# Optimization experiments

Measured on AMD Instinct MI355X. Metric: run time of the kernel, lower is better.

Reference implementation:

```python
import jax, jax.numpy as jnp
import numpy as np

NEG = -1e30  # log-space 'zero'


def setup_inputs() -> dict:
    key = jax.random.key(0)
    T, B, C, L = 1000, 32, 2000, 100
    k1, k2 = jax.random.split(key)
    activations = jax.random.normal(k1, (T, B, C), dtype=jnp.float32)
    # targets cannot be blank (blank == 0) -> sample in [1, C)
    targets = jax.random.randint(k2, (B * L,), 1, C, dtype=jnp.int32)
    input_lengths = jnp.full((B,), T, dtype=jnp.int32)
    target_lengths = jnp.full((B,), L, dtype=jnp.int32)
    return {"activations": activations, "targets": targets,
            "input_lengths": input_lengths, "target_lengths": target_lengths}


def _ctc_costs(activations, targets, input_lengths, target_lengths, blank=0):
    """Per-utterance CTC negative log likelihoods via the alpha DP recursion."""
    T, B, C = activations.shape
    L = targets.shape[0] // B  # equal label lengths per utterance (concatenated flat)
    S = 2 * L + 1              # extended label sequence: blank-interleaved
    lp = jax.nn.log_softmax(activations, axis=-1)  # [T,B,C]
    tgt = targets.reshape(B, L)
    ext = jnp.full((B, S), blank, dtype=tgt.dtype).at[:, 1::2].set(tgt)  # [B,S]
    # log-prob of each extended-label symbol at each frame: [T,B,S]
    lp_ext = jnp.take_along_axis(lp, jnp.broadcast_to(ext[None], (T, B, S)), axis=2)
    # skip transition s-2 -> s allowed iff ext[s] != blank and ext[s] != ext[s-2]
    ext_m2 = jnp.concatenate([jnp.full((B, 2), -1, ext.dtype), ext[:, :-2]], axis=1)
    skip = (ext != blank) & (ext != ext_m2)  # [B,S]

    alpha0 = (jnp.full((B, S), NEG, jnp.float32)
              .at[:, 0].set(lp_ext[0, :, 0])
              .at[:, 1].set(lp_ext[0, :, 1]))

    def step(alpha, lp_t):
        a1 = jnp.concatenate([jnp.full((B, 1), NEG, alpha.dtype), alpha[:, :-1]], axis=1)
        a2 = jnp.concatenate([jnp.full((B, 2), NEG, alpha.dtype), alpha[:, :-2]], axis=1)
        a2 = jnp.where(skip, a2, NEG)
        m = jnp.maximum(jnp.maximum(alpha, a1), a2)
        new = m + jnp.log(jnp.exp(alpha - m) + jnp.exp(a1 - m) + jnp.exp(a2 - m)) + lp_t
        return new, new

    _, alphas = jax.lax.scan(step, alpha0, lp_ext[1:])
    alphas = jnp.concatenate([alpha0[None], alphas], axis=0)  # [T,B,S]
    # alpha at the last valid frame of each utterance
    alpha_fin = alphas[input_lengths - 1, jnp.arange(B)]  # [B,S]
    s_last = (2 * target_lengths).astype(jnp.int32)  # final blank position
    a_b = jnp.take_along_axis(alpha_fin, s_last[:, None], axis=1)[:, 0]
    a_l = jnp.take_along_axis(alpha_fin, (s_last - 1)[:, None], axis=1)[:, 0]
    m = jnp.maximum(a_b, a_l)
    return -(m + jnp.log(jnp.exp(a_b - m) + jnp.exp(a_l - m)))  # [B]


def reference(activations, targets, input_lengths, target_lengths):
    # warp-ctc 'mean' reduction: sum(costs) / minibatch / sum(target_lengths)
    costs = _ctc_costs(activations, targets, input_lengths, target_lengths, blank=0)
    B = costs.shape[0]
    return jnp.sum(costs) / B / jnp.sum(target_lengths).astype(jnp.float32)
```

## Files before the change

### kernel.cpp

```cpp
#include <hip/hip_runtime.h>
#include <math.h>


#define BLK 256

__global__ __launch_bounds__(BLK) void k_lse_gather(
    const float* __restrict__ act, const int* __restrict__ targets,
    float* __restrict__ p_ext, int T, int B, int C, int L, int S)
{
  int row = blockIdx.x;
  int b = row % B;
  int t = row / B;
  int tid = threadIdx.x;
  const float* rp = act + (size_t)row * (size_t)C;
  const float4* rp4 = (const float4*)rp;
  int C4 = C >> 2;

  float4 x0 = (tid < C4) ? rp4[tid] : make_float4(-3e38f, -3e38f, -3e38f, -3e38f);
  bool h2 = (tid + BLK) < C4;
  float4 x1 = h2 ? rp4[tid + BLK] : make_float4(0.f, 0.f, 0.f, 0.f);
  float m = fmaxf(fmaxf(x0.x, x0.y), fmaxf(x0.z, x0.w));
  if (h2) m = fmaxf(m, fmaxf(fmaxf(x1.x, x1.y), fmaxf(x1.z, x1.w)));
  for (int i = tid + 2 * BLK; i < C4; i += BLK) {
    float4 x = rp4[i];
    m = fmaxf(m, fmaxf(fmaxf(x.x, x.y), fmaxf(x.z, x.w)));
  }
  #pragma unroll
  for (int o = 32; o > 0; o >>= 1) m = fmaxf(m, __shfl_xor(m, o));
  __shared__ float sm[BLK / 64];
  __shared__ float ss[BLK / 64];
  int w = tid >> 6, ln = tid & 63;
  if (ln == 0) sm[w] = m;
  __syncthreads();
  float M = fmaxf(fmaxf(sm[0], sm[1]), fmaxf(sm[2], sm[3]));

  float ssum = 0.f;
  if (tid < C4)
    ssum += expf(x0.x - M) + expf(x0.y - M) + expf(x0.z - M) + expf(x0.w - M);
  if (h2)
    ssum += expf(x1.x - M) + expf(x1.y - M) + expf(x1.z - M) + expf(x1.w - M);
  for (int i = tid + 2 * BLK; i < C4; i += BLK) {
    float4 x = rp4[i];
    ssum += expf(x.x - M) + expf(x.y - M) + expf(x.z - M) + expf(x.w - M);
  }
  #pragma unroll
  for (int o = 32; o > 0; o >>= 1) ssum += __shfl_xor(ssum, o);
  if (ln == 0) ss[w] = ssum;
  __syncthreads();
  float lse = M + logf(ss[0] + ss[1] + ss[2] + ss[3]);

  float* op = p_ext + ((size_t)b * T + t) * 256;
  float p = 0.f;
  if (tid < S) {
    int c = (tid & 1) ? targets[b * L + (tid >> 1)] : 0;
    p = expf(rp[c] - lse);
  }
  op[tid] = p;
}

__device__ __forceinline__ float wave_max64(float x) {
  int t;
  t = __builtin_amdgcn_update_dpp(0, __float_as_int(x), 0x111, 0xF, 0xF, true);
  x = fmaxf(x, __int_as_float(t));
  t = __builtin_amdgcn_update_dpp(0, __float_as_int(x), 0x112, 0xF, 0xF, true);
  x = fmaxf(x, __int_as_float(t));
  t = __builtin_amdgcn_update_dpp(0, __float_as_int(x), 0x114, 0xF, 0xF, true);
  x = fmaxf(x, __int_as_float(t));
  t = __builtin_amdgcn_update_dpp(0, __float_as_int(x), 0x118, 0xF, 0xF, true);
  x = fmaxf(x, __int_as_float(t));
  t = __builtin_amdgcn_update_dpp(0, __float_as_int(x), 0x142, 0xA, 0xF, false);
  x = fmaxf(x, __int_as_float(t));
  t = __builtin_amdgcn_update_dpp(0, __float_as_int(x), 0x143, 0xC, 0xF, false);
  x = fmaxf(x, __int_as_float(t));
  return __int_as_float(__builtin_amdgcn_readlane(__float_as_int(x), 63));
}

__device__ __forceinline__ float shift_up1(float x) {
  int t = __builtin_amdgcn_update_dpp(0, __float_as_int(x), 0x138, 0xF, 0xF, true);
  return __int_as_float(t);
}

__global__ __launch_bounds__(64, 1) void k_alpha(
    const float* __restrict__ p_ext, const int* __restrict__ targets,
    const int* __restrict__ ilen, const int* __restrict__ tlen,
    double* __restrict__ costs, int T, int B, int L)
{
  int b = blockIdx.x;
  int l = threadIdx.x;
  int Tb = ilen[b];
  int Lb = tlen[b];
  int S = 2 * Lb + 1;

  const float4* pb4 = (const float4*)(p_ext + (size_t)b * (size_t)T * 256);

  const int* tg = targets + b * L;
  float kf3 = 0.f, kf5 = 0.f, kf7 = 0.f;
  {
    int s;
    s = 4 * l - 1; if (s >= 3 && s < S) { int mm = (s - 1) >> 1; kf3 = (tg[mm] != tg[mm - 1]) ? 1.f : 0.f; }
    s = 4 * l + 1; if (s >= 3 && s < S) { int mm = (s - 1) >> 1; kf5 = (tg[mm] != tg[mm - 1]) ? 1.f : 0.f; }
    s = 4 * l + 3; if (s >= 3 && s < S) { int mm = (s - 1) >> 1; kf7 = (tg[mm] != tg[mm - 1]) ? 1.f : 0.f; }
  }

  const float BIAS = 18446744073709551616.0f;
  float a0 = 0.f, a1 = 0.f, a2 = 0.f, a3 = 0.f;
  {
    float4 p0 = pb4[l];
    if (l == 0) { a0 = p0.x * BIAS; a1 = p0.y * BIAS; }
  }
  int E = -64;

  int i0 = (l == 0) ? 0 : (l - 1);

  const int PF = 8;
  int NE = (Tb - 1) >> 1;
  int tmax = T - 2;
  float4 fa[PF], fb[PF], fc[PF];
  #pragma unroll
  for (int j = 0; j < PF; j++) {
    int t0 = 1 + 2 * j;
    t0 = (t0 > tmax) ? tmax : t0;
    fa[j] = pb4[(size_t)t0 * 64 + i0];
    fb[j] = pb4[(size_t)t0 * 64 + l];
    fc[j] = pb4[(size_t)(t0 + 1) * 64 + l];
  }

  int e = 0;
  while (e < NE) {
    #pragma unroll
    for (int j = 0; j < PF; j++) {
      int eg = e + j;
      if (eg < NE) {
        float4 Pa = fa[j], Pb = fb[j], Pc = fc[j];
        {
          int tn = 1 + 2 * (eg + PF);
          tn = (tn > tmax) ? tmax : tn;
          fa[j] = pb4[(size_t)tn * 64 + i0];
          fb[j] = pb4[(size_t)tn * 64 + l];
          fc[j] = pb4[(size_t)(tn + 1) * 64 + l];
        }

        float w0 = shift_up1(a0), w1 = shift_up1(a1);
        float w2 = shift_up1(a2), w3 = shift_up1(a3);
        float w4 = a0, w5 = a1, w6 = a2, w7 = a3;

        w7 = (w7 + w6 + kf7 * w5) * Pb.w;
        w6 = (w6 + w5) * Pb.z;
        w5 = (w5 + w4 + kf5 * w3) * Pb.y;
        w4 = (w4 + w3) * Pb.x;
        w3 = (w3 + w2 + kf3 * w1) * Pa.w;
        w2 = (w2 + w1) * Pa.z;
        w7 = (w7 + w6 + kf7 * w5) * Pc.w;
        w6 = (w6 + w5) * Pc.z;
        w5 = (w5 + w4 + kf5 * w3) * Pc.y;
        w4 = (w4 + w3) * Pc.x;
        a0 = w4; a1 = w5; a2 = w6; a3 = w7;

        if ((j & 1) == 1) {
          float mx = fmaxf(fmaxf(a0, a1), fmaxf(a2, a3));
          float Mx = wave_max64(mx);
          int ee = ilogbf(fmaxf(Mx, 1.17549435e-38f)) - 64;
          float sc = ldexpf(1.0f, -ee);
          a0 *= sc; a1 *= sc; a2 *= sc; a3 *= sc;
          E += ee;
        }
      }
    }
    e += PF;
  }

  int t = 1 + 2 * NE;
  if (t < Tb) {
    float4 P = pb4[(size_t)t * 64 + l];
    float u3 = shift_up1(a3);
    float n0 = (a0 + u3) * P.x;
    float n1 = (a1 + a0 + kf5 * u3) * P.y;
    float n2 = (a2 + a1) * P.z;
    float n3 = (a3 + a2 + kf7 * a1) * P.w;
    a0 = n0; a1 = n1; a2 = n2; a3 = n3;
  }

  __shared__ float sA[260];
  sA[4 * l + 0] = a0; sA[4 * l + 1] = a1;
  sA[4 * l + 2] = a2; sA[4 * l + 3] = a3;
  __syncthreads();
  if (l == 0) {
    double ab = (double)sA[2 * Lb];
    double al_ = (double)sA[2 * Lb - 1];
    costs[b] = -(log(ab + al_) + (double)E * 0.6931471805599453);
  }
}

__global__ __launch_bounds__(64) void k_final(
    const double* __restrict__ costs, const int* __restrict__ tlen,
    float* __restrict__ out, int B)
{
  int i = threadIdx.x;
  double c = (i < B) ? costs[i] : 0.0;
  double tl = (i < B) ? (double)tlen[i] : 0.0;
  #pragma unroll
  for (int o = 32; o > 0; o >>= 1) {
    c += __shfl_xor(c, o);
    tl += __shfl_xor(tl, o);
  }
  if (i == 0) out[0] = (float)(c / (double)B / tl);
}

extern "C" void kernel_launch(void* const* d_in, const int* in_sizes, int n_in,
                              void* d_out, int out_size, void* d_ws, size_t ws_size,
                              hipStream_t stream) {
  const float* act     = (const float*)d_in[0];
  const int*   targets = (const int*)d_in[1];
  const int*   ilen    = (const int*)d_in[2];
  const int*   tlen    = (const int*)d_in[3];
  float* out = (float*)d_out;

  int B = in_sizes[2];
  int L = in_sizes[1] / B;
  const int T = 1000, C = 2000;
  int S = 2 * L + 1;

  float* p_ext = (float*)d_ws;
  double* costs = (double*)(p_ext + (size_t)B * T * 256);

  k_lse_gather<<<T * B, BLK, 0, stream>>>(act, targets, p_ext, T, B, C, L, S);
  k_alpha<<<B, 64, 0, stream>>>(p_ext, targets, ilen, tlen, costs, T, B, L);
  k_final<<<1, 64, 0, stream>>>(costs, tlen, out, B);
}
```

Baseline: 502.3 us.

## Stream alpha-recursion inputs through an LDS ring via async global-to-LDS loads

Replaces the register-prefetch scheme in the serial alpha kernel with a 50-slot LDS ring filled by global_load_lds instructions issued 48 frames ahead, using manual vmcnt waits. The previous-lane probabilities are now obtained by shifting this lane's own values with DPP instead of a separate misaligned global load, which removes one of three loads per step. The goal is to hide global memory latency more deeply on the latency-bound sequential recursion. It relies on hand-written vmcnt counts and on the ordering of LDS-direct loads, which is fragile if the compiler emits other memory operations.

After: 476.5 us. -5.1%, faster.

```diff
diff --git a/kernel.cpp b/kernel.cpp
--- a/kernel.cpp
+++ b/kernel.cpp
@@ -3,6 +3,10 @@
 
 
 #define BLK 256
+#define RING 50
+#define AHEAD 48
+
+typedef float f32x4 __attribute__((ext_vector_type(4)));
 
 __global__ __launch_bounds__(BLK) void k_lse_gather(
     const float* __restrict__ act, const int* __restrict__ targets,
@@ -80,18 +84,28 @@
   return __int_as_float(t);
 }
 
+__device__ __forceinline__ void gload_lds16(const float* g, float* l) {
+  __builtin_amdgcn_global_load_lds(
+      (const __attribute__((address_space(1))) void*)(const void*)g,
+      (__attribute__((address_space(3))) void*)(void*)l, 16, 0, 0);
+}
+
 __global__ __launch_bounds__(64, 1) void k_alpha(
     const float* __restrict__ p_ext, const int* __restrict__ targets,
     const int* __restrict__ ilen, const int* __restrict__ tlen,
     double* __restrict__ costs, int T, int B, int L)
 {
+  __shared__ float ring[RING * 256];
+  __shared__ float sA[260];
+
   int b = blockIdx.x;
   int l = threadIdx.x;
   int Tb = ilen[b];
   int Lb = tlen[b];
   int S = 2 * Lb + 1;
 
-  const float4* pb4 = (const float4*)(p_ext + (size_t)b * (size_t)T * 256);
+  const float* pbase = p_ext + (size_t)b * (size_t)T * 256;
+  const float4* pb4 = (const float4*)pbase;
 
   const int* tg = targets + b * L;
   float kf3 = 0.f, kf5 = 0.f, kf7 = 0.f;
@@ -110,64 +124,60 @@
   }
   int E = -64;
 
-  int i0 = (l == 0) ? 0 : (l - 1);
-
-  const int PF = 8;
   int NE = (Tb - 1) >> 1;
-  int tmax = T - 2;
-  float4 fa[PF], fb[PF], fc[PF];
-  #pragma unroll
-  for (int j = 0; j < PF; j++) {
-    int t0 = 1 + 2 * j;
-    t0 = (t0 > tmax) ? tmax : t0;
-    fa[j] = pb4[(size_t)t0 * 64 + i0];
-    fb[j] = pb4[(size_t)t0 * 64 + l];
-    fc[j] = pb4[(size_t)(t0 + 1) * 64 + l];
-  }
-
-  int e = 0;
-  while (e < NE) {
-    #pragma unroll
-    for (int j = 0; j < PF; j++) {
-      int eg = e + j;
-      if (eg < NE) {
-        float4 Pa = fa[j], Pb = fb[j], Pc = fc[j];
-        {
-          int tn = 1 + 2 * (eg + PF);
-          tn = (tn > tmax) ? tmax : tn;
-          fa[j] = pb4[(size_t)tn * 64 + i0];
-          fb[j] = pb4[(size_t)tn * 64 + l];
-          fc[j] = pb4[(size_t)(tn + 1) * 64 + l];
-        }
-
-        float w0 = shift_up1(a0), w1 = shift_up1(a1);
-        float w2 = shift_up1(a2), w3 = shift_up1(a3);
-        float w4 = a0, w5 = a1, w6 = a2, w7 = a3;
-
-        w7 = (w7 + w6 + kf7 * w5) * Pb.w;
-        w6 = (w6 + w5) * Pb.z;
-        w5 = (w5 + w4 + kf5 * w3) * Pb.y;
-        w4 = (w4 + w3) * Pb.x;
-        w3 = (w3 + w2 + kf3 * w1) * Pa.w;
-        w2 = (w2 + w1) * Pa.z;
-        w7 = (w7 + w6 + kf7 * w5) * Pc.w;
-        w6 = (w6 + w5) * Pc.z;
-        w5 = (w5 + w4 + kf5 * w3) * Pc.y;
-        w4 = (w4 + w3) * Pc.x;
-        a0 = w4; a1 = w5; a2 = w6; a3 = w7;
-
-        if ((j & 1) == 1) {
-          float mx = fmaxf(fmaxf(a0, a1), fmaxf(a2, a3));
-          float Mx = wave_max64(mx);
-          int ee = ilogbf(fmaxf(Mx, 1.17549435e-38f)) - 64;
-          float sc = ldexpf(1.0f, -ee);
-          a0 *= sc; a1 *= sc; a2 *= sc; a3 *= sc;
-          E += ee;
-        }
-      }
+  int tmax = T - 1;
+
+  for (int r = 1; r <= AHEAD; ++r) {
+    int tr = (r > tmax) ? tmax : r;
+    gload_lds16(pbase + (size_t)tr * 256 + 4 * l, &ring[(r - 1) * 256]);
+  }
+
+  asm volatile("s_waitcnt vmcnt(46)" ::: "memory");
+  f32x4 Pb = *(const f32x4*)&ring[0 * 256 + 4 * l];
+  f32x4 Pc = *(const f32x4*)&ring[1 * 256 + 4 * l];
+
+  int sr = 2;
+  int si = AHEAD;
+  for (int e = 0; e < NE; ++e) {
+    asm volatile("s_waitcnt vmcnt(44)" ::: "memory");
+    f32x4 Nb = *(const f32x4*)&ring[sr * 256 + 4 * l];
+    f32x4 Nc = *(const f32x4*)&ring[sr * 256 + 256 + 4 * l];
+    {
+      int t1 = 49 + 2 * e; if (t1 > tmax) t1 = tmax;
+      int t2 = 50 + 2 * e; if (t2 > tmax) t2 = tmax;
+      gload_lds16(pbase + (size_t)t1 * 256 + 4 * l, &ring[si * 256]);
+      gload_lds16(pbase + (size_t)t2 * 256 + 4 * l, &ring[si * 256 + 256]);
     }
-    e += PF;
-  }
+    sr += 2; if (sr >= RING) sr = 0;
+    si += 2; if (si >= RING) si = 0;
+
+    float paz = shift_up1(Pb.z), paw = shift_up1(Pb.w);
+    float w1 = shift_up1(a1), w2 = shift_up1(a2), w3 = shift_up1(a3);
+    float w4 = a0, w5 = a1, w6 = a2, w7 = a3;
+    w7 = (w7 + w6 + kf7 * w5) * Pb.w;
+    w6 = (w6 + w5) * Pb.z;
+    w5 = (w5 + w4 + kf5 * w3) * Pb.y;
+    w4 = (w4 + w3) * Pb.x;
+    w3 = (w3 + w2 + kf3 * w1) * paw;
+    w2 = (w2 + w1) * paz;
+    w7 = (w7 + w6 + kf7 * w5) * Pc.w;
+    w6 = (w6 + w5) * Pc.z;
+    w5 = (w5 + w4 + kf5 * w3) * Pc.y;
+    w4 = (w4 + w3) * Pc.x;
+    a0 = w4; a1 = w5; a2 = w6; a3 = w7;
+
+    if (e & 1) {
+      float mx = fmaxf(fmaxf(a0, a1), fmaxf(a2, a3));
+      float Mx = wave_max64(mx);
+      int ee = ilogbf(fmaxf(Mx, 1.17549435e-38f)) - 64;
+      float sc = ldexpf(1.0f, -ee);
+      a0 *= sc; a1 *= sc; a2 *= sc; a3 *= sc;
+      E += ee;
+    }
+
+    Pb = Nb; Pc = Nc;
+  }
+  asm volatile("s_waitcnt vmcnt(0)" ::: "memory");
 
   int t = 1 + 2 * NE;
   if (t < Tb) {
@@ -180,7 +190,6 @@
     a0 = n0; a1 = n1; a2 = n2; a3 = n3;
   }
 
-  __shared__ float sA[260];
   sA[4 * l + 0] = a0; sA[4 * l + 1] = a1;
   sA[4 * l + 2] = a2; sA[4 * l + 3] = a3;
   __syncthreads();
```
